# Optimization experiments

Hardware: AMD Instinct MI355X
Metric: run time of the kernel (lower is better)

The kernel has to match this reference:

```python
import jax, jax.numpy as jnp
import numpy as np

OBS = 128; N_AGENT = 16; N_ACTION = 8; N_LAYER = 2; HID = 128
GE = 256; LE = 256; F1 = 512; F2 = 512


def _edges(batch_size, n):
    # all ordered pairs (i, j), i != j, within each sample; GCNConv adds self-loops
    i, j = np.meshgrid(np.arange(n), np.arange(n), indexing='ij')
    m = i != j
    src0, dst0 = i[m], j[m]                      # [n*(n-1)]
    off = (np.arange(batch_size) * n)[:, None]
    src = (src0[None, :] + off).reshape(-1)
    dst = (dst0[None, :] + off).reshape(-1)
    return jnp.asarray(src, jnp.int32), jnp.asarray(dst, jnp.int32)


def setup_inputs() -> dict:
    key = jax.random.key(0)
    ks = jax.random.split(key, 16)
    g = lambda k, shp, fan: jax.random.normal(k, shp, jnp.float32) / np.sqrt(fan)
    return {
        'obs_j': jax.random.normal(ks[0], (2048, N_AGENT, OBS), jnp.float32),
        'W_pre': g(ks[1], (OBS, HID), OBS), 'b_pre': jnp.zeros((HID,), jnp.float32),
        'W_gcn': g(ks[2], (N_LAYER, HID, HID), HID), 'b_gcn': jnp.zeros((N_LAYER, HID), jnp.float32),
        'W_post': g(ks[3], (HID, GE), HID), 'b_post': jnp.zeros((GE,), jnp.float32),
        'W_loc': g(ks[4], (OBS, LE), OBS), 'b_loc': jnp.zeros((LE,), jnp.float32),
        'W1': g(ks[5], (GE + LE, F1), GE + LE), 'b1': jnp.zeros((F1,), jnp.float32),
        'W2': g(ks[6], (F1, F2), F1), 'b2': jnp.zeros((F2,), jnp.float32),
        'W3': g(ks[7], (F2, N_ACTION), F2), 'b3': jnp.zeros((N_ACTION,), jnp.float32),
    }


def reference(obs_j, W_pre, b_pre, W_gcn, b_gcn, W_post, b_post,
              W_loc, b_loc, W1, b1, W2, b2, W3, b3):
    B, n, _ = obs_j.shape
    N = B * n
    obs = obs_j.reshape(N, OBS)
    x = jax.nn.relu(obs @ W_pre + b_pre)          # [N, HID]

    src, dst = _edges(B, n)
    # GCNConv with self-loops on a fully-connected graph: deg = n for every node,
    # edge norm = 1/sqrt(deg_i*deg_j) = 1/n for every (A+I) edge.
    inv_n = jnp.float32(1.0) / n
    for l in range(N_LAYER):
        h = x @ W_gcn[l]                          # lin (no bias inside propagate)
        agg = jax.ops.segment_sum(h[src], dst, num_segments=N)  # neighbor gather/scatter
        x = jax.nn.relu((agg + h) * inv_n + b_gcn[l])            # + self-loop msg, bias

    g = x.reshape(B, n, HID).mean(axis=1)         # global_mean_pool over each graph
    g = jax.nn.relu(g @ W_post + b_post)          # [B, GE]
    loc = jax.nn.relu(obs @ W_loc + b_loc)        # [B*n, LE]
    gi = jnp.repeat(g, n, axis=0)                 # repeat_interleave over agents
    z = jnp.concatenate([gi, loc], axis=1)
    z = jax.nn.relu(z @ W1 + b1)
    z = jax.nn.relu(z @ W2 + b2)
    q = z @ W3 + b3
    return q.reshape(B, n, N_ACTION)
```

## Files before the change

### kernel.cpp

```cpp
#include <hip/hip_runtime.h>
#include <hip/hip_bf16.h>
#include <stdint.h>

typedef __bf16 bf16;
typedef __bf16 bf16x4 __attribute__((ext_vector_type(4)));
typedef __bf16 bf16x8 __attribute__((ext_vector_type(8)));
typedef float f32x4 __attribute__((ext_vector_type(4)));

#define MFMA(a, b, c) __builtin_amdgcn_mfma_f32_16x16x32_bf16(a, b, c, 0, 0, 0)
#define GL(p) ((const __attribute__((address_space(1))) void*)(p))
#define SH(p) ((__attribute__((address_space(3))) void*)(p))

__device__ inline void tp(const float* W, bf16* WT, int id, int shiftK, int N) {
  int K = 1 << shiftK;
  int n = id >> shiftK;
  int k = id & (K - 1);
  WT[id] = (bf16)W[(size_t)k * N + n];
}

__global__ __launch_bounds__(256) void prep_all(
    const float* __restrict__ Wpre, const float* __restrict__ Wloc,
    const float* __restrict__ Wgcn, const float* __restrict__ Wpost,
    bf16* __restrict__ WpreLocT, bf16* __restrict__ Wg0T, bf16* __restrict__ Wg1T,
    bf16* __restrict__ WpostT,
    const float* __restrict__ bpre, const float* __restrict__ bloc,
    float* __restrict__ biasPL) {
  int blk = blockIdx.x;
  int tid = threadIdx.x;
  if (blk < 448) {
    int id = blk * 256 + tid;
    if (id < 16384) { tp(Wpre, WpreLocT, id, 7, 128); return; } id -= 16384;
    if (id < 32768) { tp(Wloc, WpreLocT + 16384, id, 7, 256); return; } id -= 32768;
    if (id < 16384) { tp(Wgcn, Wg0T, id, 7, 128); return; } id -= 16384;
    if (id < 16384) { tp(Wgcn + 16384, Wg1T, id, 7, 128); return; } id -= 16384;
    tp(Wpost, WpostT, id, 7, 256);
    return;
  }
  if (tid < 128) biasPL[tid] = bpre[tid];
  biasPL[128 + tid] = bloc[tid];
}

__global__ __launch_bounds__(256, 4) void k1c(
    const float* __restrict__ obs, const bf16* __restrict__ WpreLocT,
    const float* __restrict__ biasPL,
    const bf16* __restrict__ Wg0T, const bf16* __restrict__ Wg1T,
    const bf16* __restrict__ WpostT, const float* __restrict__ b_gcn,
    const float* __restrict__ b_post,
    bf16* __restrict__ gB, bf16* __restrict__ loc,
    const float* __restrict__ W1, const float* __restrict__ W2,
    bf16* __restrict__ W1T, bf16* __restrict__ W2T,
    const float* __restrict__ W3, bf16* __restrict__ W3bT,
    float* __restrict__ outq) {
  __shared__ bf16 smem[16384];

  const int tid = threadIdx.x;
  int id = blockIdx.x;

  if (id >= 768) {
    int blk = id - 768;
    if (blk < 128) {
      bf16* tile = smem;
      const float* W = (blk < 64) ? W1 : W2;
      bf16* WT = (blk < 64) ? W1T : W2T;
      int t = blk & 63;
      int tk0 = (t >> 3) * 64, tn0 = (t & 7) * 64;
#pragma unroll
      for (int p = 0; p < 4; p++) {
        int kr = p * 16 + (tid >> 4), nc = (tid & 15) * 4;
        float4 f = *(const float4*)(W + (size_t)(tk0 + kr) * 512 + tn0 + nc);
        bf16x4 v; v[0] = (bf16)f.x; v[1] = (bf16)f.y; v[2] = (bf16)f.z; v[3] = (bf16)f.w;
        *(bf16x4*)&tile[kr * 68 + nc] = v;
      }
      __syncthreads();
#pragma unroll
      for (int p = 0; p < 4; p++) {
        int nr = p * 16 + (tid >> 4), kc = (tid & 15) * 4;
        bf16x4 v;
#pragma unroll
        for (int i = 0; i < 4; i++) v[i] = tile[(kc + i) * 68 + nr];
        *(bf16x4*)(WT + (size_t)(tn0 + nr) * 512 + tk0 + kc) = v;
      }
      return;
    }
    blk -= 128;
    if (blk == 0) {
#pragma unroll
      for (int i = 0; i < 32; i++) {
        int id2 = i * 256 + tid;
        int n = id2 >> 9, k = id2 & 511;
        float w = (n < 8) ? W3[(size_t)k * 8 + n] : 0.f;
        bf16 hi = (bf16)w;
        W3bT[id2] = hi;
        W3bT[8192 + id2] = (bf16)(w - (float)hi);
      }
      return;
    }
    blk -= 1;
    float4 z = {0.f, 0.f, 0.f, 0.f};
#pragma unroll
    for (int i = 0; i < 4; i++)
      ((float4*)outq)[(size_t)blk * 1024 + i * 256 + tid] = z;
    return;
  }

  const int s = id >> 3;
  const int n_idx = s % 3;
  const int m0 = ((id & 7) + 8 * (s / 3)) * 128;
  const int n0 = n_idx * 128;

  f32x4 acc[4][4] = {};
  const int lane = tid & 63, wave = tid >> 6;
  const int wm = (wave >> 1) * 64, wn = (wave & 1) * 64;
  const int lm = lane & 15, quad = lane >> 4;

  float4 pa[4];

  auto loadA = [&](int kt) {
#pragma unroll
    for (int it = 0; it < 2; it++) {
      int idx = it * 256 + tid;
      int row = idx >> 2;
      int c = idx & 3;
      int cv = c ^ ((row >> 1) & 3);
      const float* src = obs + (size_t)(m0 + row) * 128 + kt * 32 + cv * 8;
      pa[it * 2] = *(const float4*)src;
      pa[it * 2 + 1] = *(const float4*)(src + 4);
    }
  };
  auto stageB = [&](int kt, int buf) {
    bf16* Bd = smem + buf * 8192 + 4096;
#pragma unroll
    for (int it = 0; it < 2; it++) {
      int idx = it * 256 + tid;
      int row = idx >> 2;
      int c = idx & 3;
      int cv = c ^ ((row >> 1) & 3);
      const bf16* gb = WpreLocT + (size_t)(n0 + row) * 128 + kt * 32 + cv * 8;
      __builtin_amdgcn_global_load_lds(GL(gb), SH(&Bd[(idx & ~63) * 8]), 16, 0, 0);
    }
  };
  auto commitA = [&](int buf) {
    bf16* Ad = smem + buf * 8192;
#pragma unroll
    for (int it = 0; it < 2; it++) {
      int idx = it * 256 + tid;
      int row = idx >> 2;
      int c = idx & 3;
      float4 f0 = pa[it * 2], f1 = pa[it * 2 + 1];
      bf16x8 v;
      v[0] = (bf16)f0.x; v[1] = (bf16)f0.y; v[2] = (bf16)f0.z; v[3] = (bf16)f0.w;
      v[4] = (bf16)f1.x; v[5] = (bf16)f1.y; v[6] = (bf16)f1.z; v[7] = (bf16)f1.w;
      *(bf16x8*)&Ad[row * 32 + c * 8] = v;
    }
  };
  auto compute = [&](int buf) {
    const bf16* Ar = smem + buf * 8192;
    const bf16* Br = smem + buf * 8192 + 4096;
    bf16x8 a[4], b[4];
#pragma unroll
    for (int i = 0; i < 4; i++) {
      int r = wm + lm + i * 16;
      a[i] = *(const bf16x8*)&Ar[r * 32 + ((quad ^ ((r >> 1) & 3)) * 8)];
    }
#pragma unroll
    for (int j = 0; j < 4; j++) {
      int r = wn + lm + j * 16;
      b[j] = *(const bf16x8*)&Br[r * 32 + ((quad ^ ((r >> 1) & 3)) * 8)];
    }
#pragma unroll
    for (int i = 0; i < 4; i++)
#pragma unroll
      for (int j = 0; j < 4; j++)
        acc[i][j] = MFMA(a[i], b[j], acc[i][j]);
  };

  loadA(0); stageB(0, 0); commitA(0);
  __syncthreads();
#pragma unroll
  for (int i = 0; i < 4; ++i) {
    if (i + 1 < 4) { loadA(i + 1); stageB(i + 1, (i + 1) & 1); }
    compute(i & 1);
    if (i + 1 < 4) commitA((i + 1) & 1);
    __syncthreads();
  }

  if (n_idx == 0) {
    bf16* xs = smem;
    bf16* x2 = smem + 2176;
    bf16* gS = smem + 4352;
#pragma unroll
    for (int i = 0; i < 4; i++) {
      int sl = (wave >> 1) * 4 + i;
#pragma unroll
      for (int j = 0; j < 4; j++) {
        int col = wn + j * 16 + lm;
        float bb = biasPL[col];
        float v = 0.f;
#pragma unroll
        for (int r = 0; r < 4; r++) v += fmaxf(acc[i][j][r] + bb, 0.f);
        v += __shfl_xor(v, 16);
        v += __shfl_xor(v, 32);
        if (quad == 0) xs[sl * 136 + col] = (bf16)(v * 0.0625f);
        else if (quad == 1) xs[(8 + sl) * 136 + col] = (bf16)0.f;
      }
    }
    __syncthreads();
    {
      f32x4 c2[2] = {};
#pragma unroll
      for (int ku = 0; ku < 4; ++ku) {
        bf16x8 a = *(const bf16x8*)&xs[lm * 136 + (ku * 4 + quad) * 8];
#pragma unroll
        for (int jn = 0; jn < 2; ++jn) {
          int col = (wave * 2 + jn) * 16 + lm;
          bf16x8 b = *(const bf16x8*)&Wg0T[(size_t)col * 128 + ku * 32 + quad * 8];
          c2[jn] = MFMA(a, b, c2[jn]);
        }
      }
      __syncthreads();
#pragma unroll
      for (int jn = 0; jn < 2; ++jn) {
        int col = (wave * 2 + jn) * 16 + lm;
        float bb = b_gcn[col];
#pragma unroll
        for (int r = 0; r < 4; ++r)
          x2[(quad * 4 + r) * 136 + col] = (bf16)fmaxf(c2[jn][r] + bb, 0.f);
      }
    }
    __syncthreads();
    {
      f32x4 c2[2] = {};
#pragma unroll
      for (int ku = 0; ku < 4; ++ku) {
        bf16x8 a = *(const bf16x8*)&x2[lm * 136 + (ku * 4 + quad) * 8];
#pragma unroll
        for (int jn = 0; jn < 2; ++jn) {
          int col = (wave * 2 + jn) * 16 + lm;
          bf16x8 b = *(const bf16x8*)&Wg1T[(size_t)col * 128 + ku * 32 + quad * 8];
          c2[jn] = MFMA(a, b, c2[jn]);
        }
      }
      __syncthreads();
#pragma unroll
      for (int jn = 0; jn < 2; ++jn) {
        int col = (wave * 2 + jn) * 16 + lm;
        float bb = b_gcn[128 + col];
#pragma unroll
        for (int r = 0; r < 4; ++r)
          xs[(quad * 4 + r) * 136 + col] = (bf16)fmaxf(c2[jn][r] + bb, 0.f);
      }
    }
    __syncthreads();
    {
      f32x4 c3[4] = {};
#pragma unroll
      for (int ku = 0; ku < 4; ++ku) {
        bf16x8 a = *(const bf16x8*)&xs[lm * 136 + (ku * 4 + quad) * 8];
#pragma unroll
        for (int jn = 0; jn < 4; ++jn) {
          int col = (wave * 4 + jn) * 16 + lm;
          bf16x8 b = *(const bf16x8*)&WpostT[(size_t)col * 128 + ku * 32 + quad * 8];
          c3[jn] = MFMA(a, b, c3[jn]);
        }
      }
#pragma unroll
      for (int jn = 0; jn < 4; ++jn) {
        int col = (wave * 4 + jn) * 16 + lm;
        float bb = b_post[col];
#pragma unroll
        for (int r = 0; r < 4; ++r)
          gS[(quad * 4 + r) * 264 + col] = (bf16)fmaxf(c3[jn][r] + bb, 0.f);
      }
    }
    __syncthreads();
    {
      int sample0 = m0 >> 4;
      int row = tid >> 5, col8 = (tid & 31) * 8;
      *(bf16x8*)&gB[(size_t)(sample0 + row) * 256 + col8] =
          *(const bf16x8*)&gS[row * 264 + col8];
    }
  } else {
#pragma unroll
    for (int i = 0; i < 4; i++)
#pragma unroll
      for (int j = 0; j < 4; j++) {
        int col = wn + j * 16 + lm;
        float bb = biasPL[n0 + col];
#pragma unroll
        for (int r = 0; r < 4; r++) {
          int row = wm + i * 16 + quad * 4 + r;
          smem[row * 128 + col] = (bf16)fmaxf(acc[i][j][r] + bb, 0.f);
        }
      }
    __syncthreads();
    const int coff = n0 - 128;
#pragma unroll
    for (int c = 0; c < 8; c++) {
      int ci = c * 256 + tid;
      int row = ci >> 4, col8 = (ci & 15) * 8;
      *(bf16x8*)&loc[(size_t)(m0 + row) * 256 + coff + col8] = *(const bf16x8*)&smem[row * 128 + col8];
    }
  }
}

__global__ __launch_bounds__(256, 4) void h_k(
    const bf16* __restrict__ gB, const bf16* __restrict__ W1T,
    const float* __restrict__ b1, float* __restrict__ hB) {
  __shared__ bf16 smem[16384];
  const int tid = threadIdx.x;
  const int id = blockIdx.x;
  const int n_idx = id & 3;
  const int m0 = (id >> 2) * 128;
  const int n0 = n_idx * 128;

  f32x4 acc[4][4] = {};
  const int lane = tid & 63, wave = tid >> 6;
  const int wm = (wave >> 1) * 64, wn = (wave & 1) * 64;
  const int lm = lane & 15, quad = lane >> 4;

  auto stage = [&](int kt, int buf) {
    bf16* Ad = smem + buf * 8192;
    bf16* Bd = smem + buf * 8192 + 4096;
    int k0 = kt * 32;
#pragma unroll
    for (int it = 0; it < 2; it++) {
      int idx = it * 256 + tid;
      int row = idx >> 2;
      int c = idx & 3;
      int cv = c ^ ((row >> 1) & 3);
      int kk = k0 + cv * 8;
      const bf16* ga = gB + (size_t)(m0 + row) * 256 + kk;
      __builtin_amdgcn_global_load_lds(GL(ga), SH(&Ad[(idx & ~63) * 8]), 16, 0, 0);
      const bf16* gb = W1T + (size_t)(n0 + row) * 512 + kk;
      __builtin_amdgcn_global_load_lds(GL(gb), SH(&Bd[(idx & ~63) * 8]), 16, 0, 0);
    }
  };
  auto compute = [&](int buf) {
    const bf16* Ar = smem + buf * 8192;
    const bf16* Br = smem + buf * 8192 + 4096;
    bf16x8 a[4], b[4];
#pragma unroll
    for (int i = 0; i < 4; i++) {
      int r = wm + lm + i * 16;
      a[i] = *(const bf16x8*)&Ar[r * 32 + ((quad ^ ((r >> 1) & 3)) * 8)];
    }
#pragma unroll
    for (int j = 0; j < 4; j++) {
      int r = wn + lm + j * 16;
      b[j] = *(const bf16x8*)&Br[r * 32 + ((quad ^ ((r >> 1) & 3)) * 8)];
    }
#pragma unroll
    for (int i = 0; i < 4; i++)
#pragma unroll
      for (int j = 0; j < 4; j++)
        acc[i][j] = MFMA(a[i], b[j], acc[i][j]);
  };

  stage(0, 0);
  __syncthreads();
#pragma unroll 2
  for (int i = 0; i < 8; ++i) {
    if (i + 1 < 8) stage(i + 1, (i + 1) & 1);
    compute(i & 1);
    __syncthreads();
  }

#pragma unroll
  for (int i = 0; i < 4; i++)
#pragma unroll
    for (int j = 0; j < 4; j++) {
      int col = n0 + wn + j * 16 + lm;
      float bb = b1[col];
#pragma unroll
      for (int r = 0; r < 4; r++) {
        int row = m0 + wm + i * 16 + quad * 4 + r;
        hB[(size_t)row * 512 + col] = acc[i][j][r] + bb;
      }
    }
}

template <bool HREP>
__global__ __launch_bounds__(256, 4) void gemm_k(
    const bf16* __restrict__ Ab, const bf16* __restrict__ BT,
    const float* __restrict__ bias, const float* __restrict__ hrep,
    bf16* __restrict__ C,
    const bf16* __restrict__ W3bT, const float* __restrict__ b3,
    float* __restrict__ outq) {
  __shared__ bf16 smem[16384];

  const int tid = threadIdx.x;
  const int id = blockIdx.x;
  const int s = id >> 3;
  const int n_idx = s & 3;
  const int m0 = ((id & 7) + 8 * (s >> 2)) * 128;
  const int n0 = n_idx * 128;

  f32x4 acc[4][4] = {};
  const int lane = tid & 63, wave = tid >> 6;
  const int wm = (wave >> 1) * 64, wn = (wave & 1) * 64;
  const int lm = lane & 15, quad = lane >> 4;

  auto stage = [&](int kt, int buf) {
    bf16* Ad = smem + buf * 8192;
    bf16* Bd = smem + buf * 8192 + 4096;
    int k0 = kt * 32;
#pragma unroll
    for (int it = 0; it < 2; it++) {
      int idx = it * 256 + tid;
      int row = idx >> 2;
      int c = idx & 3;
      int cv = c ^ ((row >> 1) & 3);
      int kk = k0 + cv * 8;
      const bf16* ga = HREP ? (Ab + (size_t)(m0 + row) * 256 + kk)
                            : (Ab + (size_t)(m0 + row) * 512 + kk);
      __builtin_amdgcn_global_load_lds(GL(ga), SH(&Ad[(idx & ~63) * 8]), 16, 0, 0);
      const bf16* gb = HREP ? (BT + (size_t)(n0 + row) * 512 + 256 + kk)
                            : (BT + (size_t)(n0 + row) * 512 + kk);
      __builtin_amdgcn_global_load_lds(GL(gb), SH(&Bd[(idx & ~63) * 8]), 16, 0, 0);
    }
  };

  auto compute = [&](int buf) {
    const bf16* Ar = smem + buf * 8192;
    const bf16* Br = smem + buf * 8192 + 4096;
    bf16x8 a[4], b[4];
#pragma unroll
    for (int i = 0; i < 4; i++) {
      int r = wm + lm + i * 16;
      a[i] = *(const bf16x8*)&Ar[r * 32 + ((quad ^ ((r >> 1) & 3)) * 8)];
    }
#pragma unroll
    for (int j = 0; j < 4; j++) {
      int r = wn + lm + j * 16;
      b[j] = *(const bf16x8*)&Br[r * 32 + ((quad ^ ((r >> 1) & 3)) * 8)];
    }
#pragma unroll
    for (int i = 0; i < 4; i++)
#pragma unroll
      for (int j = 0; j < 4; j++)
        acc[i][j] = MFMA(a[i], b[j], acc[i][j]);
  };

  const int NIT = HREP ? 8 : 16;
  stage(0, 0);
  __syncthreads();
#pragma unroll 2
  for (int i = 0; i < NIT; ++i) {
    if (i + 1 < NIT) stage(i + 1, (i + 1) & 1);
    compute(i & 1);
    __syncthreads();
  }

  if (HREP) {
#pragma unroll
    for (int i = 0; i < 4; i++) {
      int sample = (m0 + wm + i * 16) >> 4;
#pragma unroll
      for (int j = 0; j < 4; j++) {
        int col = n0 + wn + j * 16 + lm;
        float hv = hrep[(size_t)sample * 512 + col];
#pragma unroll
        for (int r = 0; r < 4; r++) {
          int row = wm + i * 16 + quad * 4 + r;
          smem[row * 128 + (col - n0)] = (bf16)fmaxf(acc[i][j][r] + hv, 0.f);
        }
      }
    }
    __syncthreads();
#pragma unroll
    for (int c = 0; c < 8; c++) {
      int ci = c * 256 + tid;
      int row = ci >> 4, col8 = (ci & 15) * 8;
      *(bf16x8*)&C[(size_t)(m0 + row) * 512 + n0 + col8] = *(const bf16x8*)&smem[row * 128 + col8];
    }
  } else {
#pragma unroll
    for (int i = 0; i < 4; i++)
#pragma unroll
      for (int j = 0; j < 4; j++) {
        int col = wn + j * 16 + lm;
        float bb = bias[n0 + col];
#pragma unroll
        for (int r = 0; r < 4; r++) {
          int row = wm + i * 16 + quad * 4 + r;
          int pc = (col >> 3) ^ (row & 7);
          smem[row * 128 + pc * 8 + (col & 7)] = (bf16)fmaxf(acc[i][j][r] + bb, 0.f);
        }
      }
    __syncthreads();
    bf16x8 w3h[4], w3l[4];
#pragma unroll
    for (int kt = 0; kt < 4; kt++) {
      w3h[kt] = *(const bf16x8*)&W3bT[lm * 512 + n0 + kt * 32 + quad * 8];
      w3l[kt] = *(const bf16x8*)&W3bT[8192 + lm * 512 + n0 + kt * 32 + quad * 8];
    }
    f32x4 qacc[2] = {};
#pragma unroll
    for (int it = 0; it < 2; it++)
#pragma unroll
      for (int kt = 0; kt < 4; kt++) {
        int rr = wave * 32 + it * 16 + lm;
        bf16x8 a = *(const bf16x8*)&smem[rr * 128 + (((kt * 4 + quad) ^ (rr & 7)) * 8)];
        qacc[it] = MFMA(a, w3h[kt], qacc[it]);
        qacc[it] = MFMA(a, w3l[kt], qacc[it]);
      }
    float qb = (n_idx == 0 && lm < 8) ? b3[lm] : 0.f;
    if (lm < 8) {
#pragma unroll
      for (int it = 0; it < 2; it++)
#pragma unroll
        for (int r = 0; r < 4; r++) {
          int row = m0 + wave * 32 + it * 16 + quad * 4 + r;
          atomicAdd(&outq[(size_t)row * 8 + lm], qacc[it][r] + qb);
        }
    }
  }
}

extern "C" void kernel_launch(void* const* d_in, const int* in_sizes, int n_in,
                              void* d_out, int out_size, void* d_ws, size_t ws_size,
                              hipStream_t stream) {
  const float* obs    = (const float*)d_in[0];
  const float* W_pre  = (const float*)d_in[1];
  const float* b_pre  = (const float*)d_in[2];
  const float* W_gcn  = (const float*)d_in[3];
  const float* b_gcn  = (const float*)d_in[4];
  const float* W_post = (const float*)d_in[5];
  const float* b_post = (const float*)d_in[6];
  const float* W_loc  = (const float*)d_in[7];
  const float* b_loc  = (const float*)d_in[8];
  const float* W1     = (const float*)d_in[9];
  const float* b1     = (const float*)d_in[10];
  const float* W2     = (const float*)d_in[11];
  const float* b2     = (const float*)d_in[12];
  const float* W3     = (const float*)d_in[13];
  const float* b3     = (const float*)d_in[14];
  float* out = (float*)d_out;

  char* p = (char*)d_ws;
  auto alloc = [&](size_t bytes) { char* r = p; p += (bytes + 255) & ~(size_t)255; return r; };
  bf16* WpreLocT = (bf16*)alloc(384 * 128 * 2);
  float* biasPL  = (float*)alloc(384 * 4);
  bf16* Wg0T   = (bf16*)alloc(128 * 128 * 2);
  bf16* Wg1T   = (bf16*)alloc(128 * 128 * 2);
  bf16* WpostT = (bf16*)alloc(256 * 128 * 2);
  bf16* W1T    = (bf16*)alloc(512 * 512 * 2);
  bf16* W2T    = (bf16*)alloc(512 * 512 * 2);
  bf16* W3bT   = (bf16*)alloc(2 * 16 * 512 * 2);
  bf16* gB     = (bf16*)alloc((size_t)2048 * 256 * 2);
  bf16* locB   = (bf16*)alloc((size_t)32768 * 256 * 2);
  float* hB    = (float*)alloc((size_t)2048 * 512 * 4);
  bf16* z1B    = (bf16*)alloc((size_t)32768 * 512 * 2);

  prep_all<<<449, 256, 0, stream>>>(W_pre, W_loc, W_gcn, W_post,
                                    WpreLocT, Wg0T, Wg1T, WpostT,
                                    b_pre, b_loc, biasPL);
  k1c<<<961, 256, 0, stream>>>(obs, WpreLocT, biasPL,
                               Wg0T, Wg1T, WpostT, b_gcn, b_post,
                               gB, locB,
                               W1, W2, W1T, W2T, W3, W3bT, out);
  h_k<<<64, 256, 0, stream>>>(gB, W1T, b1, hB);
  gemm_k<true><<<1024, 256, 0, stream>>>(locB, W1T, nullptr, hB, z1B,
                                         nullptr, nullptr, nullptr);
  gemm_k<false><<<1024, 256, 0, stream>>>(z1B, W2T, b2, nullptr, nullptr,
                                          W3bT, b3, out);
}
```

Before: 151.6 us.

## Replace W2/W3 GEMM with 256x256-tile 8-wave kernel using phased pipelining

```diff
diff --git a/kernel.cpp b/kernel.cpp
--- a/kernel.cpp
+++ b/kernel.cpp
@@ -10,6 +10,9 @@
 #define MFMA(a, b, c) __builtin_amdgcn_mfma_f32_16x16x32_bf16(a, b, c, 0, 0, 0)
 #define GL(p) ((const __attribute__((address_space(1))) void*)(p))
 #define SH(p) ((__attribute__((address_space(3))) void*)(p))
+#define BARRIER() do { __builtin_amdgcn_s_barrier(); asm volatile("" ::: "memory"); } while (0)
+#define WAIT_LGKM0() do { asm volatile("s_waitcnt lgkmcnt(0)" ::: "memory"); __builtin_amdgcn_sched_barrier(0); } while (0)
+#define WAIT_VM(N) do { asm volatile("s_waitcnt vmcnt(" #N ")" ::: "memory"); __builtin_amdgcn_sched_barrier(0); } while (0)
 
 __device__ inline void tp(const float* W, bf16* WT, int id, int shiftK, int N) {
   int K = 1 << shiftK;
@@ -411,11 +414,9 @@
       int c = idx & 3;
       int cv = c ^ ((row >> 1) & 3);
       int kk = k0 + cv * 8;
-      const bf16* ga = HREP ? (Ab + (size_t)(m0 + row) * 256 + kk)
-                            : (Ab + (size_t)(m0 + row) * 512 + kk);
+      const bf16* ga = Ab + (size_t)(m0 + row) * 256 + kk;
       __builtin_amdgcn_global_load_lds(GL(ga), SH(&Ad[(idx & ~63) * 8]), 16, 0, 0);
-      const bf16* gb = HREP ? (BT + (size_t)(n0 + row) * 512 + 256 + kk)
-                            : (BT + (size_t)(n0 + row) * 512 + kk);
+      const bf16* gb = BT + (size_t)(n0 + row) * 512 + 256 + kk;
       __builtin_amdgcn_global_load_lds(GL(gb), SH(&Bd[(idx & ~63) * 8]), 16, 0, 0);
     }
   };
@@ -441,7 +442,7 @@
         acc[i][j] = MFMA(a[i], b[j], acc[i][j]);
   };
 
-  const int NIT = HREP ? 8 : 16;
+  const int NIT = 8;
   stage(0, 0);
   __syncthreads();
 #pragma unroll 2
@@ -451,69 +452,179 @@
     __syncthreads();
   }
 
-  if (HREP) {
+#pragma unroll
+  for (int i = 0; i < 4; i++) {
+    int sample = (m0 + wm + i * 16) >> 4;
+#pragma unroll
+    for (int j = 0; j < 4; j++) {
+      int col = n0 + wn + j * 16 + lm;
+      float hv = hrep[(size_t)sample * 512 + col];
+#pragma unroll
+      for (int r = 0; r < 4; r++) {
+        int row = wm + i * 16 + quad * 4 + r;
+        smem[row * 128 + (col - n0)] = (bf16)fmaxf(acc[i][j][r] + hv, 0.f);
+      }
+    }
+  }
+  __syncthreads();
+#pragma unroll
+  for (int c = 0; c < 8; c++) {
+    int ci = c * 256 + tid;
+    int row = ci >> 4, col8 = (ci & 15) * 8;
+    *(bf16x8*)&C[(size_t)(m0 + row) * 512 + n0 + col8] = *(const bf16x8*)&smem[row * 128 + col8];
+  }
+}
+
+__global__ __launch_bounds__(512, 1) void k4_8ph(
+    const bf16* __restrict__ Ab, const bf16* __restrict__ W2T,
+    const float* __restrict__ b2, const bf16* __restrict__ W3bT,
+    const float* __restrict__ b3, float* __restrict__ outq) {
+  __shared__ bf16 smem[65536];
+
+  const int tid = threadIdx.x;
+  const int id = blockIdx.x;
+  const int n_idx = id >> 7;
+  const int m0 = (id & 127) * 256;
+  const int n0 = n_idx * 256;
+
+  f32x4 acc[8][4] = {};
+  const int lane = tid & 63, wave = tid >> 6;
+  const int wm = (wave >> 2) * 128, wn = (wave & 3) * 64;
+  const int lm = lane & 15, quad = lane >> 4;
+
+  auto stageH = [&](int t, int m, int kh, int buf) {
+    bf16* D = smem + buf * 32768 + m * 16384 + kh * 8192;
+    const bf16* S = m ? W2T : Ab;
+    int rbase = m ? n0 : m0;
+#pragma unroll
+    for (int it = 0; it < 2; it++) {
+      int idx = it * 512 + tid;
+      int row = idx >> 2;
+      int c = idx & 3;
+      int cv = c ^ ((row >> 1) & 3);
+      const bf16* g = S + (size_t)(rbase + row) * 512 + t * 64 + kh * 32 + cv * 8;
+      __builtin_amdgcn_global_load_lds(GL(g), SH(&D[(idx & ~63) * 8]), 16, 0, 0);
+    }
+  };
+  auto dsrA = [&](bf16x8* a, int buf, int ihalf, int kh) {
+    const bf16* Ar = smem + buf * 32768 + kh * 8192;
 #pragma unroll
     for (int i = 0; i < 4; i++) {
-      int sample = (m0 + wm + i * 16) >> 4;
-#pragma unroll
-      for (int j = 0; j < 4; j++) {
-        int col = n0 + wn + j * 16 + lm;
-        float hv = hrep[(size_t)sample * 512 + col];
-#pragma unroll
-        for (int r = 0; r < 4; r++) {
-          int row = wm + i * 16 + quad * 4 + r;
-          smem[row * 128 + (col - n0)] = (bf16)fmaxf(acc[i][j][r] + hv, 0.f);
-        }
-      }
-    }
-    __syncthreads();
-#pragma unroll
-    for (int c = 0; c < 8; c++) {
-      int ci = c * 256 + tid;
-      int row = ci >> 4, col8 = (ci & 15) * 8;
-      *(bf16x8*)&C[(size_t)(m0 + row) * 512 + n0 + col8] = *(const bf16x8*)&smem[row * 128 + col8];
-    }
-  } else {
+      int r = wm + lm + (ihalf * 4 + i) * 16;
+      a[i] = *(const bf16x8*)&Ar[r * 32 + ((quad ^ ((r >> 1) & 3)) * 8)];
+    }
+  };
+  auto dsrB = [&](bf16x8* b, int buf, int kh) {
+    const bf16* Br = smem + buf * 32768 + 16384 + kh * 8192;
+#pragma unroll
+    for (int j = 0; j < 4; j++) {
+      int r = wn + lm + j * 16;
+      b[j] = *(const bf16x8*)&Br[r * 32 + ((quad ^ ((r >> 1) & 3)) * 8)];
+    }
+  };
+  auto mfma16 = [&](bf16x8* a, bf16x8* b, int ihalf) {
+    __builtin_amdgcn_s_setprio(1);
 #pragma unroll
     for (int i = 0; i < 4; i++)
 #pragma unroll
-      for (int j = 0; j < 4; j++) {
-        int col = wn + j * 16 + lm;
-        float bb = bias[n0 + col];
-#pragma unroll
-        for (int r = 0; r < 4; r++) {
-          int row = wm + i * 16 + quad * 4 + r;
-          int pc = (col >> 3) ^ (row & 7);
-          smem[row * 128 + pc * 8 + (col & 7)] = (bf16)fmaxf(acc[i][j][r] + bb, 0.f);
-        }
-      }
-    __syncthreads();
-    bf16x8 w3h[4], w3l[4];
-#pragma unroll
-    for (int kt = 0; kt < 4; kt++) {
-      w3h[kt] = *(const bf16x8*)&W3bT[lm * 512 + n0 + kt * 32 + quad * 8];
-      w3l[kt] = *(const bf16x8*)&W3bT[8192 + lm * 512 + n0 + kt * 32 + quad * 8];
-    }
-    f32x4 qacc[2] = {};
+      for (int j = 0; j < 4; j++)
+        acc[ihalf * 4 + i][j] = MFMA(a[i], b[j], acc[ihalf * 4 + i][j]);
+    __builtin_amdgcn_s_setprio(0);
+  };
+
+  stageH(0, 0, 0, 0); stageH(0, 1, 0, 0); stageH(0, 0, 1, 0); stageH(0, 1, 1, 0);
+  WAIT_VM(4);
+  BARRIER();
+
+  const int NT = 8;
+  for (int t = 0; t < NT - 1; ++t) {
+    int cur = t & 1, nxt = cur ^ 1;
+    bf16x8 a[4], b[4];
+    dsrA(a, cur, 0, 0); dsrB(b, cur, 0);
+    stageH(t + 1, 0, 0, nxt);
+    BARRIER(); WAIT_LGKM0();
+    mfma16(a, b, 0);
+    BARRIER();
+    dsrA(a, cur, 1, 0);
+    stageH(t + 1, 1, 0, nxt);
+    WAIT_VM(4);
+    BARRIER(); WAIT_LGKM0();
+    mfma16(a, b, 1);
+    BARRIER();
+    dsrA(a, cur, 0, 1); dsrB(b, cur, 1);
+    stageH(t + 1, 0, 1, nxt);
+    BARRIER(); WAIT_LGKM0();
+    mfma16(a, b, 0);
+    BARRIER();
+    dsrA(a, cur, 1, 1);
+    stageH(t + 1, 1, 1, nxt);
+    WAIT_VM(4);
+    BARRIER(); WAIT_LGKM0();
+    mfma16(a, b, 1);
+    BARRIER();
+  }
+  {
+    const int cur = (NT - 1) & 1;
+    bf16x8 a[4], b[4];
+    dsrA(a, cur, 0, 0); dsrB(b, cur, 0);
+    BARRIER(); WAIT_LGKM0();
+    mfma16(a, b, 0);
+    BARRIER();
+    dsrA(a, cur, 1, 0);
+    WAIT_VM(0);
+    BARRIER(); WAIT_LGKM0();
+    mfma16(a, b, 1);
+    BARRIER();
+    dsrA(a, cur, 0, 1); dsrB(b, cur, 1);
+    BARRIER(); WAIT_LGKM0();
+    mfma16(a, b, 0);
+    BARRIER();
+    dsrA(a, cur, 1, 1);
+    BARRIER(); WAIT_LGKM0();
+    mfma16(a, b, 1);
+    BARRIER();
+  }
+
+  __syncthreads();
+#pragma unroll
+  for (int i = 0; i < 8; i++)
+#pragma unroll
+    for (int j = 0; j < 4; j++) {
+      int col = wn + j * 16 + lm;
+      float bb = b2[n0 + col];
+#pragma unroll
+      for (int r = 0; r < 4; r++) {
+        int row = wm + i * 16 + quad * 4 + r;
+        int pc = (col >> 3) ^ (row & 7);
+        smem[row * 256 + pc * 8 + (col & 7)] = (bf16)fmaxf(acc[i][j][r] + bb, 0.f);
+      }
+    }
+  __syncthreads();
+  bf16x8 w3h[8], w3l[8];
+#pragma unroll
+  for (int kt = 0; kt < 8; kt++) {
+    w3h[kt] = *(const bf16x8*)&W3bT[lm * 512 + n0 + kt * 32 + quad * 8];
+    w3l[kt] = *(const bf16x8*)&W3bT[8192 + lm * 512 + n0 + kt * 32 + quad * 8];
+  }
+  f32x4 qacc[2] = {};
+#pragma unroll
+  for (int it = 0; it < 2; it++)
+#pragma unroll
+    for (int kt = 0; kt < 8; kt++) {
+      int rr = wave * 32 + it * 16 + lm;
+      bf16x8 a = *(const bf16x8*)&smem[rr * 256 + (((kt * 4 + quad) ^ (rr & 7)) * 8)];
+      qacc[it] = MFMA(a, w3h[kt], qacc[it]);
+      qacc[it] = MFMA(a, w3l[kt], qacc[it]);
+    }
+  float qb = (n_idx == 0 && lm < 8) ? b3[lm] : 0.f;
+  if (lm < 8) {
 #pragma unroll
     for (int it = 0; it < 2; it++)
 #pragma unroll
-      for (int kt = 0; kt < 4; kt++) {
-        int rr = wave * 32 + it * 16 + lm;
-        bf16x8 a = *(const bf16x8*)&smem[rr * 128 + (((kt * 4 + quad) ^ (rr & 7)) * 8)];
-        qacc[it] = MFMA(a, w3h[kt], qacc[it]);
-        qacc[it] = MFMA(a, w3l[kt], qacc[it]);
-      }
-    float qb = (n_idx == 0 && lm < 8) ? b3[lm] : 0.f;
-    if (lm < 8) {
-#pragma unroll
-      for (int it = 0; it < 2; it++)
-#pragma unroll
-        for (int r = 0; r < 4; r++) {
-          int row = m0 + wave * 32 + it * 16 + quad * 4 + r;
-          atomicAdd(&outq[(size_t)row * 8 + lm], qacc[it][r] + qb);
-        }
-    }
+      for (int r = 0; r < 4; r++) {
+        int row = m0 + wave * 32 + it * 16 + quad * 4 + r;
+        atomicAdd(&outq[(size_t)row * 8 + lm], qacc[it][r] + qb);
+      }
   }
 }
 
@@ -562,6 +673,5 @@
   h_k<<<64, 256, 0, stream>>>(gB, W1T, b1, hB);
   gemm_k<true><<<1024, 256, 0, stream>>>(locB, W1T, nullptr, hB, z1B,
                                          nullptr, nullptr, nullptr);
-  gemm_k<false><<<1024, 256, 0, stream>>>(z1B, W2T, b2, nullptr, nullptr,
-                                          W3bT, b3, out);
+  k4_8ph<<<256, 512, 0, stream>>>(z1B, W2T, b2, W3bT, b3, out);
 }
```

Result: faster. 148.2 us (-2.3%).
